# Kernel tuning notes

Hardware: AMD Instinct MI355X
Metric: run time of the kernel (lower is better)

## Reference

```python
import jax, jax.numpy as jnp
import numpy as np
import math

TIN = 4          # patch_size
NF = 128         # num_features
DM = 256         # d_model
NH = 8           # n_heads
HD = DM // NH    # head_dim = 32
FF = 1024        # ff_dim
NL = 4           # num_layers
MAXD = 64        # max_rel_dist -> L = 129


def _ln(x, g, b, eps):
    mu = jnp.mean(x, axis=-1, keepdims=True)
    var = jnp.mean(jnp.square(x - mu), axis=-1, keepdims=True)
    return (x - mu) * jax.lax.rsqrt(var + eps) * g + b


def setup_inputs() -> dict:
    key = jax.random.key(0)
    ks = jax.random.split(key, 24)
    s = 0.02
    d = {
        'x': jax.random.normal(ks[0], (2000, 16, NF), jnp.float32),
        'ln1_g': jnp.ones((TIN * NF,), jnp.float32),
        'ln1_b': jnp.zeros((TIN * NF,), jnp.float32),
        'proj_w': jax.random.normal(ks[1], (TIN * NF, DM), jnp.float32) * s,
        'proj_b': jnp.zeros((DM,), jnp.float32),
        'ln2_g': jnp.ones((DM,), jnp.float32),
        'ln2_b': jnp.zeros((DM,), jnp.float32),
        'rel_bias': jax.random.normal(ks[2], (NH, 2 * MAXD + 1), jnp.float32) * s,
        'ln_attn_g': jnp.ones((NL, DM), jnp.float32),
        'ln_attn_b': jnp.zeros((NL, DM), jnp.float32),
        'qkv_w': jax.random.normal(ks[3], (NL, DM, 3 * DM), jnp.float32) * s,
        'qkv_b': jnp.zeros((NL, 3 * DM), jnp.float32),
        'out_w': jax.random.normal(ks[4], (NL, DM, DM), jnp.float32) * s,
        'out_b': jnp.zeros((NL, DM), jnp.float32),
        'ln_ff_g': jnp.ones((NL, DM), jnp.float32),
        'ln_ff_b': jnp.zeros((NL, DM), jnp.float32),
        'ff1_w': jax.random.normal(ks[5], (NL, DM, FF), jnp.float32) * s,
        'ff1_b': jnp.zeros((NL, FF), jnp.float32),
        'ff2_w': jax.random.normal(ks[6], (NL, FF, DM), jnp.float32) * s,
        'ff2_b': jnp.zeros((NL, DM), jnp.float32),
        'fln_g': jnp.ones((DM,), jnp.float32),
        'fln_b': jnp.zeros((DM,), jnp.float32),
        'op_w': jax.random.normal(ks[7], (DM, NF), jnp.float32) * s,
        'op_b': jnp.zeros((NF,), jnp.float32),
    }
    return d


def reference(x, ln1_g, ln1_b, proj_w, proj_b, ln2_g, ln2_b, rel_bias,
              ln_attn_g, ln_attn_b, qkv_w, qkv_b, out_w, out_b,
              ln_ff_g, ln_ff_b, ff1_w, ff1_b, ff2_w, ff2_b,
              fln_g, fln_b, op_w, op_b):
    # ---- PatchEmbedding ----
    h = jnp.swapaxes(x, 0, 1)                 # [B, T, F]
    B, T, F = h.shape
    n_patch = T // TIN                        # 500 (== chunk_size, single chunk path)
    h = h[:, :n_patch * TIN, :].reshape(B, n_patch, TIN * F)
    h = _ln(h, ln1_g, ln1_b, 1e-6)
    h = h @ proj_w + proj_b
    h = _ln(h, ln2_g, ln2_b, 1e-6)            # [B, S, DM]
    S = n_patch

    # ---- relative position bias [H, S, S] ----
    pos = jnp.arange(S)
    rel = pos[None, :] - pos[:, None]
    idx = jnp.clip(rel, -MAXD, MAXD) + MAXD
    bias = rel_bias[:, idx]                   # [H, S, S]

    # ---- causal mask ----
    causal = jnp.triu(jnp.full((S, S), -jnp.inf, jnp.float32), k=1)
    scale = 1.0 / math.sqrt(HD)

    for l in range(NL):
        # attention block
        a = _ln(h, ln_attn_g[l], ln_attn_b[l], 1e-5)
        qkv = a @ qkv_w[l] + qkv_b[l]         # [B, S, 3*DM]
        q, k, v = jnp.split(qkv, 3, axis=-1)
        q = q.reshape(B, S, NH, HD)
        k = k.reshape(B, S, NH, HD)
        v = v.reshape(B, S, NH, HD)
        scores = jnp.einsum('bihd,bjhd->bhij', q, k) * scale
        scores = scores + bias[None] + causal
        attn = jax.nn.softmax(scores, axis=-1)
        o = jnp.einsum('bhij,bjhd->bihd', attn, v).reshape(B, S, DM)
        h = h + (o @ out_w[l] + out_b[l])
        # ffn block
        f = _ln(h, ln_ff_g[l], ln_ff_b[l], 1e-5)
        f = jax.nn.gelu(f @ ff1_w[l] + ff1_b[l], approximate=False)
        h = h + (f @ ff2_w[l] + ff2_b[l])

    h = _ln(h, fln_g, fln_b, 1e-5)
    h = h @ op_w + op_b                       # [B, S, NF]
    return jnp.swapaxes(h, 0, 1)              # [S, B, NF]
```

## Files before the change

kernel.cpp:

```cpp
#include <hip/hip_runtime.h>

#define TS 500
#define NB 16
#define NROW 8000
#define DMODEL 256
#define NHEAD 8
#define HDIM 32
#define FFD 1024

typedef __bf16 bf16x8 __attribute__((ext_vector_type(8)));
typedef __bf16 bf16x4 __attribute__((ext_vector_type(4)));
typedef float  f32x4  __attribute__((ext_vector_type(4)));
typedef float  f32x2  __attribute__((ext_vector_type(2)));

__device__ __forceinline__ float wred_sum(float v) {
    #pragma unroll
    for (int off = 32; off; off >>= 1) v += __shfl_xor(v, off, 64);
    return v;
}

__device__ __forceinline__ void pa_store(__bf16* __restrict__ PA, int KS,
                                         int grow, int col, float y) {
    int mt = grow >> 4, rl = grow & 15;
    size_t idx = ((size_t)(mt * KS + (col >> 5)) * 64 + ((col >> 3) & 3) * 16 + rl) * 8 + (col & 7);
    PA[idx] = (__bf16)y;
}

__device__ __forceinline__ void ya_store(__bf16* __restrict__ YA,
                                         int lrow, int col, float y) {
    int mtl = lrow >> 4, rl = lrow & 15;
    int idx = (((mtl * 8 + (col >> 5)) * 64) + ((col >> 3) & 3) * 16 + rl) * 8 + (col & 7);
    YA[idx] = (__bf16)y;
}

__global__ __launch_bounds__(256) void k_pack_all(
    const float* __restrict__ qkv_w, const float* __restrict__ out_w,
    const float* __restrict__ ff1_w, const float* __restrict__ ff2_w,
    const float* __restrict__ proj_w, const float* __restrict__ op_w,
    __bf16* __restrict__ PBq, __bf16* __restrict__ PBo,
    __bf16* __restrict__ PB1, __bf16* __restrict__ PB2,
    __bf16* __restrict__ PBp, __bf16* __restrict__ PBop)
{
    int bid = blockIdx.x;
    const float* W; __bf16* PB; int KS, NT, wLS, pLS, l, bx;
    if (bid < 384)       { W = qkv_w;  PB = PBq;  KS = 8;  NT = 48; wLS = 196608; pLS = 196608; l = bid / 96;           bx = bid % 96; }
    else if (bid < 512)  { W = out_w;  PB = PBo;  KS = 8;  NT = 16; wLS = 65536;  pLS = 65536;  l = (bid - 384) / 32;   bx = (bid - 384) % 32; }
    else if (bid < 1024) { W = ff1_w;  PB = PB1;  KS = 8;  NT = 64; wLS = 262144; pLS = 262144; l = (bid - 512) / 128;  bx = (bid - 512) % 128; }
    else if (bid < 1536) { W = ff2_w;  PB = PB2;  KS = 32; NT = 16; wLS = 262144; pLS = 262144; l = (bid - 1024) / 128; bx = (bid - 1024) % 128; }
    else if (bid < 1600) { W = proj_w; PB = PBp;  KS = 16; NT = 16; wLS = 0;      pLS = 0;      l = 0;                  bx = bid - 1536; }
    else                 { W = op_w;   PB = PBop; KS = 8;  NT = 8;  wLS = 0;      pLS = 0;      l = 0;                  bx = bid - 1600; }

    int gid = bx * 256 + threadIdx.x;
    if (gid >= NT * KS * 64) return;
    int lane = gid & 63;
    int ks = (gid >> 6) % KS;
    int nt = (gid >> 6) / KS;
    int N = NT * 16;
    int k0 = ks * 32 + (lane >> 4) * 8;
    int col = nt * 16 + (lane & 15);
    const float* src = W + (size_t)l * wLS;
    bf16x8 v;
    #pragma unroll
    for (int j = 0; j < 8; j++) v[j] = (__bf16)src[(size_t)(k0 + j) * N + col];
    *(bf16x8*)(PB + (size_t)l * pLS + ((size_t)(nt * KS + ks) * 64 + lane) * 8) = v;
}

__global__ __launch_bounds__(256) void k_patchfused(
    const float* __restrict__ x, const float* __restrict__ g1, const float* __restrict__ b1,
    const __bf16* __restrict__ PBp, const float* __restrict__ bias,
    float* __restrict__ h,
    const float* __restrict__ gam, const float* __restrict__ bet,
    const float* __restrict__ gam2, const float* __restrict__ bet2,
    const __bf16* __restrict__ PBq0, const float* __restrict__ qb0,
    __bf16* __restrict__ qkvb)
{
    __shared__ __align__(16) __bf16 As[2][16][64][8];
    __shared__ float redS[4][32];
    __shared__ float redQ[4][32];
    int t = threadIdx.x, lane = t & 63, w = t >> 6;
    int row0 = blockIdx.x * 32;

    for (int rr = 0; rr < 8; rr++) {
        int lrow = w * 8 + rr;
        int row = row0 + lrow;
        int b = row / TS, pp = row - b * TS;
        int kb = lane * 8;
        const float* src = x + ((size_t)(pp * 4 + (kb >> 7)) * NB + b) * 128 + (kb & 127);
        float4 lo = *(const float4*)src;
        float4 hi = *(const float4*)(src + 4);
        float v[8] = {lo.x, lo.y, lo.z, lo.w, hi.x, hi.y, hi.z, hi.w};
        float sm_ = 0.f;
        #pragma unroll
        for (int j = 0; j < 8; j++) sm_ += v[j];
        sm_ = wred_sum(sm_);
        float mu = sm_ * (1.0f / 512.0f);
        float q = 0.f;
        #pragma unroll
        for (int j = 0; j < 8; j++) { float d = v[j] - mu; q += d * d; }
        q = wred_sum(q);
        float rs = rsqrtf(q * (1.0f / 512.0f) + 1e-6f);
        float4 gl = *(const float4*)(g1 + kb), gh = *(const float4*)(g1 + kb + 4);
        float4 bl = *(const float4*)(b1 + kb), bh = *(const float4*)(b1 + kb + 4);
        float gg[8] = {gl.x, gl.y, gl.z, gl.w, gh.x, gh.y, gh.z, gh.w};
        float bbv[8] = {bl.x, bl.y, bl.z, bl.w, bh.x, bh.y, bh.z, bh.w};
        bf16x8 yv;
        #pragma unroll
        for (int j = 0; j < 8; j++) yv[j] = (__bf16)((v[j] - mu) * rs * gg[j] + bbv[j]);
        *(bf16x8*)&As[lrow >> 4][lane >> 2][(lane & 3) * 16 + (lrow & 15)][0] = yv;
    }
    __syncthreads();

    const bf16x8* B8 = (const bf16x8*)PBp;
    f32x4 acc[2][4] = {};
    #pragma unroll 8
    for (int ks = 0; ks < 16; ks++) {
        bf16x8 a0 = *(const bf16x8*)&As[0][ks][lane][0];
        bf16x8 a1 = *(const bf16x8*)&As[1][ks][lane][0];
        #pragma unroll
        for (int n = 0; n < 4; n++) {
            bf16x8 b = B8[((size_t)(w * 4 + n) * 16 + ks) * 64 + lane];
            acc[0][n] = __builtin_amdgcn_mfma_f32_16x16x32_bf16(a0, b, acc[0][n], 0, 0, 0);
            acc[1][n] = __builtin_amdgcn_mfma_f32_16x16x32_bf16(a1, b, acc[1][n], 0, 0, 0);
        }
    }

    int g_ = lane >> 4, cl = lane & 15;
    int rbase = g_ * 4;
    float gamv[4], betv[4], gam2v[4], bet2v[4];
    #pragma unroll
    for (int n = 0; n < 4; n++) {
        int col = (w * 4 + n) * 16 + cl;
        float bv = bias[col];
        gamv[n] = gam[col]; betv[n] = bet[col];
        gam2v[n] = gam2[col]; bet2v[n] = bet2[col];
        #pragma unroll
        for (int m = 0; m < 2; m++)
            #pragma unroll
            for (int r = 0; r < 4; r++) acc[m][n][r] += bv;
    }
    float mu[2][4], rstd[2][4];
    {
        float ps[2][4];
        #pragma unroll
        for (int m = 0; m < 2; m++)
            #pragma unroll
            for (int r = 0; r < 4; r++) {
                float s2 = acc[m][0][r] + acc[m][1][r] + acc[m][2][r] + acc[m][3][r];
                #pragma unroll
                for (int off = 1; off < 16; off <<= 1) s2 += __shfl_xor(s2, off, 64);
                ps[m][r] = s2;
            }
        if (cl == 0)
            #pragma unroll
            for (int m = 0; m < 2; m++)
                #pragma unroll
                for (int r = 0; r < 4; r++) redS[w][m * 16 + rbase + r] = ps[m][r];
        __syncthreads();
        #pragma unroll
        for (int m = 0; m < 2; m++)
            #pragma unroll
            for (int r = 0; r < 4; r++) {
                int lr = m * 16 + rbase + r;
                mu[m][r] = (redS[0][lr] + redS[1][lr] + redS[2][lr] + redS[3][lr]) * (1.0f / 256.0f);
            }
        float pq[2][4];
        #pragma unroll
        for (int m = 0; m < 2; m++)
            #pragma unroll
            for (int r = 0; r < 4; r++) {
                float s2 = 0.f;
                #pragma unroll
                for (int n = 0; n < 4; n++) { float d = acc[m][n][r] - mu[m][r]; s2 += d * d; }
                #pragma unroll
                for (int off = 1; off < 16; off <<= 1) s2 += __shfl_xor(s2, off, 64);
                pq[m][r] = s2;
            }
        if (cl == 0)
            #pragma unroll
            for (int m = 0; m < 2; m++)
                #pragma unroll
                for (int r = 0; r < 4; r++) redQ[w][m * 16 + rbase + r] = pq[m][r];
        __syncthreads();
        #pragma unroll
        for (int m = 0; m < 2; m++)
            #pragma unroll
            for (int r = 0; r < 4; r++) {
                int lr = m * 16 + rbase + r;
                float var = (redQ[0][lr] + redQ[1][lr] + redQ[2][lr] + redQ[3][lr]) * (1.0f / 256.0f);
                rstd[m][r] = rsqrtf(var + 1e-6f);
            }
    }
    float ps2[2][4];
    #pragma unroll
    for (int m = 0; m < 2; m++) {
        int row = row0 + m * 16 + rbase;
        #pragma unroll
        for (int r = 0; r < 4; r++) {
            float s2 = 0.f;
            #pragma unroll
            for (int n = 0; n < 4; n++) {
                int col = (w * 4 + n) * 16 + cl;
                float y1 = (acc[m][n][r] - mu[m][r]) * rstd[m][r] * gamv[n] + betv[n];
                h[(size_t)(row + r) * 256 + col] = y1;
                s2 += y1;
            }
            #pragma unroll
            for (int off = 1; off < 16; off <<= 1) s2 += __shfl_xor(s2, off, 64);
            ps2[m][r] = s2;
        }
    }
    if (cl == 0)
        #pragma unroll
        for (int m = 0; m < 2; m++)
            #pragma unroll
            for (int r = 0; r < 4; r++) redS[w][m * 16 + rbase + r] = ps2[m][r];
    __syncthreads();
    float mu2[2][4], rstd2[2][4];
    #pragma unroll
    for (int m = 0; m < 2; m++)
        #pragma unroll
        for (int r = 0; r < 4; r++) {
            int lr = m * 16 + rbase + r;
            mu2[m][r] = (redS[0][lr] + redS[1][lr] + redS[2][lr] + redS[3][lr]) * (1.0f / 256.0f);
        }
    float pq2[2][4];
    #pragma unroll
    for (int m = 0; m < 2; m++)
        #pragma unroll
        for (int r = 0; r < 4; r++) {
            float s2 = 0.f;
            #pragma unroll
            for (int n = 0; n < 4; n++) {
                float y1 = (acc[m][n][r] - mu[m][r]) * rstd[m][r] * gamv[n] + betv[n];
                float d = y1 - mu2[m][r];
                s2 += d * d;
            }
            #pragma unroll
            for (int off = 1; off < 16; off <<= 1) s2 += __shfl_xor(s2, off, 64);
            pq2[m][r] = s2;
        }
    if (cl == 0)
        #pragma unroll
        for (int m = 0; m < 2; m++)
            #pragma unroll
            for (int r = 0; r < 4; r++) redQ[w][m * 16 + rbase + r] = pq2[m][r];
    __syncthreads();
    #pragma unroll
    for (int m = 0; m < 2; m++)
        #pragma unroll
        for (int r = 0; r < 4; r++) {
            int lr = m * 16 + rbase + r;
            float var = (redQ[0][lr] + redQ[1][lr] + redQ[2][lr] + redQ[3][lr]) * (1.0f / 256.0f);
            rstd2[m][r] = rsqrtf(var + 1e-5f);
        }
    __bf16* YA = &As[0][0][0][0];
    #pragma unroll
    for (int m = 0; m < 2; m++) {
        #pragma unroll
        for (int n = 0; n < 4; n++) {
            int col = (w * 4 + n) * 16 + cl;
            #pragma unroll
            for (int r = 0; r < 4; r++) {
                float y1 = (acc[m][n][r] - mu[m][r]) * rstd[m][r] * gamv[n] + betv[n];
                float y2 = (y1 - mu2[m][r]) * rstd2[m][r] * gam2v[n] + bet2v[n];
                ya_store(YA, m * 16 + rbase + r, col, y2);
            }
        }
    }
    __syncthreads();

    const bf16x8* YA8 = (const bf16x8*)YA;
    const bf16x8* B8q = (const bf16x8*)PBq0;
    for (int m = 0; m < 2; m++) {
        f32x4 acc2[12] = {};
        for (int ks = 0; ks < 8; ks++) {
            bf16x8 a = YA8[(m * 8 + ks) * 64 + lane];
            #pragma unroll
            for (int n = 0; n < 12; n++) {
                bf16x8 b = B8q[((size_t)(w * 12 + n) * 8 + ks) * 64 + lane];
                acc2[n] = __builtin_amdgcn_mfma_f32_16x16x32_bf16(a, b, acc2[n], 0, 0, 0);
            }
        }
        int row = row0 + m * 16 + rbase;
        #pragma unroll
        for (int n = 0; n < 12; n++) {
            int col = (w * 12 + n) * 16 + cl;
            float bv = qb0[col];
            #pragma unroll
            for (int r = 0; r < 4; r++)
                qkvb[(size_t)(row + r) * 768 + col] = (__bf16)(acc2[n][r] + bv);
        }
    }
}

__global__ __launch_bounds__(512) void k_outproj(
    const __bf16* __restrict__ PA, const __bf16* __restrict__ PB,
    const float* __restrict__ bias, float* __restrict__ dst,
    __bf16* __restrict__ dstb,
    const float* __restrict__ gam, const float* __restrict__ bet)
{
    __shared__ float redS[8][16];
    __shared__ float redQ[8][16];
    int t = threadIdx.x, lane = t & 63, w = t >> 6;
    int mt0 = blockIdx.x;

    const bf16x8* A8 = (const bf16x8*)PA;
    const bf16x8* B8 = (const bf16x8*)PB;

    f32x4 acc[2] = {};
    #pragma unroll 8
    for (int ks = 0; ks < 8; ks++) {
        bf16x8 a = A8[((size_t)mt0 * 8 + ks) * 64 + lane];
        #pragma unroll
        for (int n = 0; n < 2; n++) {
            bf16x8 b = B8[((size_t)(w * 2 + n) * 8 + ks) * 64 + lane];
            acc[n] = __builtin_amdgcn_mfma_f32_16x16x32_bf16(a, b, acc[n], 0, 0, 0);
        }
    }

    int g_ = lane >> 4, cl = lane & 15;
    int rbase = g_ * 4;
    float gamv[2], betv[2];
    #pragma unroll
    for (int n = 0; n < 2; n++) {
        int col = (w * 2 + n) * 16 + cl;
        float bv = bias[col];
        gamv[n] = gam[col]; betv[n] = bet[col];
        int row = mt0 * 16 + rbase;
        #pragma unroll
        for (int r = 0; r < 4; r++) {
            float v = acc[n][r] + bv + dst[(size_t)(row + r) * 256 + col];
            dst[(size_t)(row + r) * 256 + col] = v;
            acc[n][r] = v;
        }
    }
    float mu[4], rstd[4];
    {
        float ps[4];
        #pragma unroll
        for (int r = 0; r < 4; r++) {
            float s2 = acc[0][r] + acc[1][r];
            #pragma unroll
            for (int off = 1; off < 16; off <<= 1) s2 += __shfl_xor(s2, off, 64);
            ps[r] = s2;
        }
        if (cl == 0)
            #pragma unroll
            for (int r = 0; r < 4; r++) redS[w][rbase + r] = ps[r];
        __syncthreads();
        #pragma unroll
        for (int r = 0; r < 4; r++) {
            int lr = rbase + r;
            float s2 = 0.f;
            #pragma unroll
            for (int ww = 0; ww < 8; ww++) s2 += redS[ww][lr];
            mu[r] = s2 * (1.0f / 256.0f);
        }
        float pq[4];
        #pragma unroll
        for (int r = 0; r < 4; r++) {
            float s2 = 0.f;
            #pragma unroll
            for (int n = 0; n < 2; n++) { float d = acc[n][r] - mu[r]; s2 += d * d; }
            #pragma unroll
            for (int off = 1; off < 16; off <<= 1) s2 += __shfl_xor(s2, off, 64);
            pq[r] = s2;
        }
        if (cl == 0)
            #pragma unroll
            for (int r = 0; r < 4; r++) redQ[w][rbase + r] = pq[r];
        __syncthreads();
        #pragma unroll
        for (int r = 0; r < 4; r++) {
            int lr = rbase + r;
            float s2 = 0.f;
            #pragma unroll
            for (int ww = 0; ww < 8; ww++) s2 += redQ[ww][lr];
            rstd[r] = rsqrtf(s2 * (1.0f / 256.0f) + 1e-5f);
        }
    }
    int row = mt0 * 16 + rbase;
    #pragma unroll
    for (int n = 0; n < 2; n++) {
        int col = (w * 2 + n) * 16 + cl;
        #pragma unroll
        for (int r = 0; r < 4; r++) {
            float y = (acc[n][r] - mu[r]) * rstd[r] * gamv[n] + betv[n];
            pa_store(dstb, 8, row + r, col, y);
        }
    }
}

template<int MODE>
__global__ __launch_bounds__(512) void k_fffused(
    const __bf16* __restrict__ PA, const __bf16* __restrict__ PB1,
    const float* __restrict__ b1, const __bf16* __restrict__ PB2,
    const float* __restrict__ b2, float* __restrict__ h,
    const float* __restrict__ gam, const float* __restrict__ bet,
    const __bf16* __restrict__ PBn, const float* __restrict__ bn,
    __bf16* __restrict__ qkvb, float* __restrict__ outp)
{
    __shared__ __align__(16) __bf16 F1T[1024][16];
    __shared__ float redS[8][16];
    __shared__ float redQ[8][16];
    int t = threadIdx.x, lane = t & 63, w = t >> 6;
    int mt = blockIdx.x;
    int g_ = lane >> 4, cl = lane & 15, rbase = g_ * 4;

    const bf16x8* A8 = (const bf16x8*)PA;
    const bf16x8* B81 = (const bf16x8*)PB1;
    const bf16x8* B82 = (const bf16x8*)PB2;

    f32x4 acc1[8] = {};
    #pragma unroll 2
    for (int ks = 0; ks < 8; ks++) {
        bf16x8 a = A8[((size_t)mt * 8 + ks) * 64 + lane];
        #pragma unroll
        for (int n = 0; n < 8; n++) {
            bf16x8 b = B81[((size_t)(w * 8 + n) * 8 + ks) * 64 + lane];
            acc1[n] = __builtin_amdgcn_mfma_f32_16x16x32_bf16(a, b, acc1[n], 0, 0, 0);
        }
    }
    #pragma unroll
    for (int n = 0; n < 8; n++) {
        int col = (w * 8 + n) * 16 + cl;
        float bv = b1[col];
        bf16x4 pv;
        #pragma unroll
        for (int r = 0; r < 4; r++) {
            float xx = acc1[n][r] + bv;
            pv[r] = (__bf16)(0.5f * xx * (1.0f + erff(xx * 0.70710678118654752f)));
        }
        *(bf16x4*)&F1T[col][rbase] = pv;
    }
    __syncthreads();

    f32x4 acc[2] = {};
    for (int kb = 0; kb < 8; kb++) {
        f32x2 lo[4], hi[4];
        #pragma unroll
        for (int q = 0; q < 4; q++) {
            unsigned ta = (unsigned)(uintptr_t)&F1T[(kb * 4 + q) * 32 + 8 * g_][0] + cl * 8;
            asm volatile("ds_read_b64_tr_b16 %0, %1" : "=v"(lo[q]) : "v"(ta) : "memory");
            asm volatile("ds_read_b64_tr_b16 %0, %1 offset:128" : "=v"(hi[q]) : "v"(ta) : "memory");
        }
        asm volatile("s_waitcnt lgkmcnt(0)" ::: "memory");
        __builtin_amdgcn_sched_barrier(0);
        #pragma unroll
        for (int q = 0; q < 4; q++) {
            int ks = kb * 4 + q;
            f32x4 pc = {lo[q][0], lo[q][1], hi[q][0], hi[q][1]};
            bf16x8 a = __builtin_bit_cast(bf16x8, pc);
            #pragma unroll
            for (int n = 0; n < 2; n++) {
                bf16x8 b = B82[((size_t)(w * 2 + n) * 32 + ks) * 64 + lane];
                acc[n] = __builtin_amdgcn_mfma_f32_16x16x32_bf16(a, b, acc[n], 0, 0, 0);
            }
        }
    }

    float gamv[2], betv[2];
    #pragma unroll
    for (int n = 0; n < 2; n++) {
        int col = (w * 2 + n) * 16 + cl;
        float bv = b2[col];
        gamv[n] = gam[col]; betv[n] = bet[col];
        int row = mt * 16 + rbase;
        #pragma unroll
        for (int r = 0; r < 4; r++) {
            float v = acc[n][r] + bv + h[(size_t)(row + r) * 256 + col];
            h[(size_t)(row + r) * 256 + col] = v;
            acc[n][r] = v;
        }
    }
    float mu[4], rstd[4];
    {
        float ps[4];
        #pragma unroll
        for (int r = 0; r < 4; r++) {
            float s2 = acc[0][r] + acc[1][r];
            #pragma unroll
            for (int off = 1; off < 16; off <<= 1) s2 += __shfl_xor(s2, off, 64);
            ps[r] = s2;
        }
        if (cl == 0)
            #pragma unroll
            for (int r = 0; r < 4; r++) redS[w][rbase + r] = ps[r];
        __syncthreads();
        #pragma unroll
        for (int r = 0; r < 4; r++) {
            int lr = rbase + r;
            float s2 = 0.f;
            #pragma unroll
            for (int ww = 0; ww < 8; ww++) s2 += redS[ww][lr];
            mu[r] = s2 * (1.0f / 256.0f);
        }
        float pq[4];
        #pragma unroll
        for (int r = 0; r < 4; r++) {
            float s2 = 0.f;
            #pragma unroll
            for (int n = 0; n < 2; n++) { float d = acc[n][r] - mu[r]; s2 += d * d; }
            #pragma unroll
            for (int off = 1; off < 16; off <<= 1) s2 += __shfl_xor(s2, off, 64);
            pq[r] = s2;
        }
        if (cl == 0)
            #pragma unroll
            for (int r = 0; r < 4; r++) redQ[w][rbase + r] = pq[r];
        __syncthreads();
        #pragma unroll
        for (int r = 0; r < 4; r++) {
            int lr = rbase + r;
            float s2 = 0.f;
            #pragma unroll
            for (int ww = 0; ww < 8; ww++) s2 += redQ[ww][lr];
            rstd[r] = rsqrtf(s2 * (1.0f / 256.0f) + 1e-5f);
        }
    }
    __bf16* YA = &F1T[0][0];
    #pragma unroll
    for (int n = 0; n < 2; n++) {
        int col = (w * 2 + n) * 16 + cl;
        #pragma unroll
        for (int r = 0; r < 4; r++) {
            float y = (acc[n][r] - mu[r]) * rstd[r] * gamv[n] + betv[n];
            ya_store(YA, rbase + r, col, y);
        }
    }
    __syncthreads();

    const bf16x8* YA8 = (const bf16x8*)YA;
    const bf16x8* B8n = (const bf16x8*)PBn;
    if constexpr (MODE == 0) {
        f32x4 acc2[6] = {};
        for (int ks = 0; ks < 8; ks++) {
            bf16x8 a = YA8[ks * 64 + lane];
            #pragma unroll
            for (int n = 0; n < 6; n++) {
                bf16x8 b = B8n[((size_t)(w * 6 + n) * 8 + ks) * 64 + lane];
                acc2[n] = __builtin_amdgcn_mfma_f32_16x16x32_bf16(a, b, acc2[n], 0, 0, 0);
            }
        }
        int row = mt * 16 + rbase;
        #pragma unroll
        for (int n = 0; n < 6; n++) {
            int col = (w * 6 + n) * 16 + cl;
            float bv = bn[col];
            #pragma unroll
            for (int r = 0; r < 4; r++)
                qkvb[(size_t)(row + r) * 768 + col] = (__bf16)(acc2[n][r] + bv);
        }
    } else {
        f32x4 acc2 = {};
        #pragma unroll 4
        for (int ks = 0; ks < 8; ks++) {
            bf16x8 a = YA8[ks * 64 + lane];
            bf16x8 b = B8n[((size_t)w * 8 + ks) * 64 + lane];
            acc2 = __builtin_amdgcn_mfma_f32_16x16x32_bf16(a, b, acc2, 0, 0, 0);
        }
        int row = mt * 16 + rbase;
        int col = w * 16 + cl;
        float bv = bn[col];
        #pragma unroll
        for (int r = 0; r < 4; r++) {
            int grow = row + r;
            int bq = grow / TS, pp = grow - bq * TS;
            outp[((size_t)pp * NB + bq) * 128 + col] = acc2[r] + bv;
        }
    }
}

__global__ __launch_bounds__(256) void k_attn(
    const __bf16* __restrict__ qkv, const float* __restrict__ rel_bias,
    __bf16* __restrict__ PA)
{
    __shared__ __align__(16) __bf16 Kfr[4][64][8];
    __shared__ __align__(16) __bf16 Vpl[2][64][16];
    __shared__ __align__(16) __bf16 PT[4][64][16];
    __shared__ float bias_s[132];

    int bh = blockIdx.x, qt = 7 - blockIdx.y;
    int b = bh >> 3, hh = bh & 7;
    int q0 = qt * 64;
    int t = threadIdx.x, lane = t & 63, w = t >> 6;
    int c = lane & 15, g = lane >> 4;

    const __bf16* base = qkv + (size_t)b * TS * 768 + hh * 32;

    if (t < 129) bias_s[t] = rel_bias[hh * 129 + t];

    bf16x8 aq = {};
    {
        int qi = q0 + 16 * w + c;
        if (qi < TS) aq = *(const bf16x8*)(base + (size_t)qi * 768 + 8 * g);
    }

    float lpart[4] = {0.f, 0.f, 0.f, 0.f};
    f32x4 O0 = {}, O1 = {};
    const float scale = 0.17677669529663687f;

    int nj = qt + 1;

    for (int it = 0; it < nj; it++) {
        int j0 = it * 64;
        __syncthreads();
        {
            int j = j0 + w * 16 + c;
            bf16x8 kv = {};
            if (j < TS) kv = *(const bf16x8*)(base + (size_t)j * 768 + 256 + 8 * g);
            *(bf16x8*)&Kfr[w][lane][0] = kv;
        }
        {
            int jl = t >> 2, dseg = t & 3;
            int j = j0 + jl;
            bf16x8 vv = {};
            if (j < TS) vv = *(const bf16x8*)(base + (size_t)j * 768 + 512 + 8 * dseg);
            *(bf16x8*)&Vpl[dseg >> 1][jl][(dseg & 1) * 8] = vv;
        }
        __syncthreads();

        f32x4 S[4];
        f32x4 zero = {};
        #pragma unroll
        for (int jt = 0; jt < 4; jt++) {
            bf16x8 bk = *(const bf16x8*)&Kfr[jt][lane][0];
            S[jt] = __builtin_amdgcn_mfma_f32_16x16x32_bf16(aq, bk, zero, 0, 0, 0);
        }

        #pragma unroll
        for (int jt = 0; jt < 4; jt++) {
            int j = j0 + jt * 16 + c;
            #pragma unroll
            for (int r = 0; r < 4; r++) {
                int i = q0 + 16 * w + 4 * g + r;
                int rel = j - i;
                rel = rel < -64 ? -64 : (rel > 64 ? 64 : rel);
                float sv = S[jt][r] * scale + bias_s[rel + 64];
                float pr = (j > i) ? 0.f : __expf(sv);
                S[jt][r] = pr;
                lpart[r] += pr;
            }
        }

        #pragma unroll
        for (int jt = 0; jt < 4; jt++) {
            bf16x4 pv;
            pv[0] = (__bf16)S[jt][0]; pv[1] = (__bf16)S[jt][1];
            pv[2] = (__bf16)S[jt][2]; pv[3] = (__bf16)S[jt][3];
            *(bf16x4*)&PT[w][jt * 16 + c][4 * g] = pv;
        }
        asm volatile("s_waitcnt lgkmcnt(0)" ::: "memory");
        __builtin_amdgcn_sched_barrier(0);

        f32x2 pa_lo[2], pa_hi[2], vb_lo[2][2], vb_hi[2][2];
        #pragma unroll
        for (int jb = 0; jb < 2; jb++) {
            unsigned pta = (unsigned)(uintptr_t)&PT[w][jb * 32 + 8 * g][0] + c * 8;
            asm volatile("ds_read_b64_tr_b16 %0, %1" : "=v"(pa_lo[jb]) : "v"(pta) : "memory");
            asm volatile("ds_read_b64_tr_b16 %0, %1 offset:128" : "=v"(pa_hi[jb]) : "v"(pta) : "memory");
            #pragma unroll
            for (int dh = 0; dh < 2; dh++) {
                unsigned vta = (unsigned)(uintptr_t)&Vpl[dh][jb * 32 + 8 * g][0] + c * 8;
                asm volatile("ds_read_b64_tr_b16 %0, %1" : "=v"(vb_lo[jb][dh]) : "v"(vta) : "memory");
                asm volatile("ds_read_b64_tr_b16 %0, %1 offset:128" : "=v"(vb_hi[jb][dh]) : "v"(vta) : "memory");
            }
        }
        asm volatile("s_waitcnt lgkmcnt(0)" ::: "memory");
        __builtin_amdgcn_sched_barrier(0);

        #pragma unroll
        for (int jb = 0; jb < 2; jb++) {
            f32x4 pc = {pa_lo[jb][0], pa_lo[jb][1], pa_hi[jb][0], pa_hi[jb][1]};
            bf16x8 pa = __builtin_bit_cast(bf16x8, pc);
            f32x4 v0c = {vb_lo[jb][0][0], vb_lo[jb][0][1], vb_hi[jb][0][0], vb_hi[jb][0][1]};
            f32x4 v1c = {vb_lo[jb][1][0], vb_lo[jb][1][1], vb_hi[jb][1][0], vb_hi[jb][1][1]};
            bf16x8 vb0 = __builtin_bit_cast(bf16x8, v0c);
            bf16x8 vb1 = __builtin_bit_cast(bf16x8, v1c);
            O0 = __builtin_amdgcn_mfma_f32_16x16x32_bf16(pa, vb0, O0, 0, 0, 0);
            O1 = __builtin_amdgcn_mfma_f32_16x16x32_bf16(pa, vb1, O1, 0, 0, 0);
        }
    }

    #pragma unroll
    for (int r = 0; r < 4; r++) {
        #pragma unroll
        for (int off = 1; off < 16; off <<= 1) lpart[r] += __shfl_xor(lpart[r], off, 64);
    }
    #pragma unroll
    for (int r = 0; r < 4; r++) {
        int i = q0 + 16 * w + 4 * g + r;
        if (i < TS) {
            float inv = 1.0f / lpart[r];
            int grow = b * TS + i;
            int mt = grow >> 4, rl = grow & 15;
            size_t fb = (size_t)(mt * 8 + hh) * 64;
            PA[(fb + ((c >> 3) & 1) * 16 + rl) * 8 + (c & 7)]       = (__bf16)(O0[r] * inv);
            PA[(fb + (2 + ((c >> 3) & 1)) * 16 + rl) * 8 + (c & 7)] = (__bf16)(O1[r] * inv);
        }
    }
}

extern "C" void kernel_launch(void* const* d_in, const int* in_sizes, int n_in,
                              void* d_out, int out_size, void* d_ws, size_t ws_size,
                              hipStream_t stream)
{
    const float* x        = (const float*)d_in[0];
    const float* ln1_g    = (const float*)d_in[1];
    const float* ln1_b    = (const float*)d_in[2];
    const float* proj_w   = (const float*)d_in[3];
    const float* proj_b   = (const float*)d_in[4];
    const float* ln2_g    = (const float*)d_in[5];
    const float* ln2_b    = (const float*)d_in[6];
    const float* rel_bias = (const float*)d_in[7];
    const float* ln_attn_g= (const float*)d_in[8];
    const float* ln_attn_b= (const float*)d_in[9];
    const float* qkv_w    = (const float*)d_in[10];
    const float* qkv_b    = (const float*)d_in[11];
    const float* out_w    = (const float*)d_in[12];
    const float* out_b    = (const float*)d_in[13];
    const float* ln_ff_g  = (const float*)d_in[14];
    const float* ln_ff_b  = (const float*)d_in[15];
    const float* ff1_w    = (const float*)d_in[16];
    const float* ff1_b    = (const float*)d_in[17];
    const float* ff2_w    = (const float*)d_in[18];
    const float* ff2_b    = (const float*)d_in[19];
    const float* fln_g    = (const float*)d_in[20];
    const float* fln_b    = (const float*)d_in[21];
    const float* op_w     = (const float*)d_in[22];
    const float* op_b     = (const float*)d_in[23];
    float* out = (float*)d_out;

    char* ws = (char*)d_ws;
    float*  h     = (float*)(ws);
    __bf16* qkvb  = (__bf16*)(ws + 8192000);
    __bf16* PA    = (__bf16*)(ws + 20480000);
    __bf16* PBq   = (__bf16*)(ws + 24576000);
    __bf16* PBo   = (__bf16*)(ws + 26148864);
    __bf16* PB1   = (__bf16*)(ws + 26673152);
    __bf16* PB2   = (__bf16*)(ws + 28770304);
    __bf16* PBp   = (__bf16*)(ws + 30867456);
    __bf16* PBop  = (__bf16*)(ws + 31129600);

    k_pack_all<<<1616, 256, 0, stream>>>(qkv_w, out_w, ff1_w, ff2_w, proj_w, op_w,
                                         PBq, PBo, PB1, PB2, PBp, PBop);

    k_patchfused<<<250, 256, 0, stream>>>(x, ln1_g, ln1_b, PBp, proj_b, h,
                                          ln2_g, ln2_b, ln_attn_g, ln_attn_b,
                                          PBq, qkv_b, qkvb);

    for (int l = 0; l < 4; l++) {
        dim3 ag(NB * NHEAD, 8);
        k_attn<<<ag, 256, 0, stream>>>(qkvb, rel_bias, PA);
        k_outproj<<<500, 512, 0, stream>>>(PA, PBo + (size_t)l * 65536, out_b + l * 256,
                                           h, PA, ln_ff_g + l * 256, ln_ff_b + l * 256);
        if (l < 3) {
            k_fffused<0><<<500, 512, 0, stream>>>(PA, PB1 + (size_t)l * 262144, ff1_b + l * 1024,
                                                  PB2 + (size_t)l * 262144, ff2_b + l * 256, h,
                                                  ln_attn_g + (l + 1) * 256, ln_attn_b + (l + 1) * 256,
                                                  PBq + (size_t)(l + 1) * 196608, qkv_b + (l + 1) * 768,
                                                  qkvb, nullptr);
        } else {
            k_fffused<1><<<500, 512, 0, stream>>>(PA, PB1 + (size_t)l * 262144, ff1_b + l * 1024,
                                                  PB2 + (size_t)l * 262144, ff2_b + l * 256, h,
                                                  fln_g, fln_b,
                                                  PBop, op_b, nullptr, out);
        }
    }
}
```

Measured before the change: 285.3 us.

## Share K/V tiles between two adjacent query tiles per attention block

Each attention block now has 512 threads covering two adjacent 64-row query tiles (pr pairs qt=2pr and 2pr+1), so every K/V tile staged in shared memory is reused by 8 waves rather than 4. The grid halves, and loading is split so waves 0-3 stage K while waves 4-7 stage V. This cuts redundant global reads of K/V and removes half the block launches. In exchange, the lower query tile idles for one iteration and the larger blocks have a coarser causal load balance.

```diff
diff --git a/kernel.cpp b/kernel.cpp
--- a/kernel.cpp
+++ b/kernel.cpp
@@ -571,19 +571,22 @@
     }
 }
 
-__global__ __launch_bounds__(256) void k_attn(
+__global__ __launch_bounds__(512) void k_attn(
     const __bf16* __restrict__ qkv, const float* __restrict__ rel_bias,
     __bf16* __restrict__ PA)
 {
     __shared__ __align__(16) __bf16 Kfr[4][64][8];
     __shared__ __align__(16) __bf16 Vpl[2][64][16];
-    __shared__ __align__(16) __bf16 PT[4][64][16];
+    __shared__ __align__(16) __bf16 PT[8][64][16];
     __shared__ float bias_s[132];
 
-    int bh = blockIdx.x, qt = 7 - blockIdx.y;
+    int bh = blockIdx.x;
+    int pr = 3 - blockIdx.y;
     int b = bh >> 3, hh = bh & 7;
-    int q0 = qt * 64;
     int t = threadIdx.x, lane = t & 63, w = t >> 6;
+    int wg = w & 3, grp = w >> 2;
+    int qt = 2 * pr + 1 - grp;
+    int q0 = qt * 64 + wg * 16;
     int c = lane & 15, g = lane >> 4;
 
     const __bf16* base = qkv + (size_t)b * TS * 768 + hh * 32;
@@ -592,7 +595,7 @@
 
     bf16x8 aq = {};
     {
-        int qi = q0 + 16 * w + c;
+        int qi = q0 + c;
         if (qi < TS) aq = *(const bf16x8*)(base + (size_t)qi * 768 + 8 * g);
     }
 
@@ -600,19 +603,19 @@
     f32x4 O0 = {}, O1 = {};
     const float scale = 0.17677669529663687f;
 
-    int nj = qt + 1;
+    int nj = 2 * pr + 2;
 
     for (int it = 0; it < nj; it++) {
         int j0 = it * 64;
         __syncthreads();
-        {
+        if (w < 4) {
             int j = j0 + w * 16 + c;
             bf16x8 kv = {};
             if (j < TS) kv = *(const bf16x8*)(base + (size_t)j * 768 + 256 + 8 * g);
             *(bf16x8*)&Kfr[w][lane][0] = kv;
-        }
-        {
-            int jl = t >> 2, dseg = t & 3;
+        } else {
+            int t2 = t - 256;
+            int jl = t2 >> 2, dseg = t2 & 3;
             int j = j0 + jl;
             bf16x8 vv = {};
             if (j < TS) vv = *(const bf16x8*)(base + (size_t)j * 768 + 512 + 8 * dseg);
@@ -620,6 +623,8 @@
         }
         __syncthreads();
 
+        if (it > qt) continue;
+
         f32x4 S[4];
         f32x4 zero = {};
         #pragma unroll
@@ -633,13 +638,13 @@
             int j = j0 + jt * 16 + c;
             #pragma unroll
             for (int r = 0; r < 4; r++) {
-                int i = q0 + 16 * w + 4 * g + r;
+                int i = q0 + 4 * g + r;
                 int rel = j - i;
                 rel = rel < -64 ? -64 : (rel > 64 ? 64 : rel);
                 float sv = S[jt][r] * scale + bias_s[rel + 64];
-                float pr = (j > i) ? 0.f : __expf(sv);
-                S[jt][r] = pr;
-                lpart[r] += pr;
+                float pr_ = (j > i) ? 0.f : __expf(sv);
+                S[jt][r] = pr_;
+                lpart[r] += pr_;
             }
         }
 
@@ -689,7 +694,7 @@
     }
     #pragma unroll
     for (int r = 0; r < 4; r++) {
-        int i = q0 + 16 * w + 4 * g + r;
+        int i = q0 + 4 * g + r;
         if (i < TS) {
             float inv = 1.0f / lpart[r];
             int grow = b * TS + i;
@@ -750,8 +755,8 @@
                                           PBq, qkv_b, qkvb);
 
     for (int l = 0; l < 4; l++) {
-        dim3 ag(NB * NHEAD, 8);
-        k_attn<<<ag, 256, 0, stream>>>(qkvb, rel_bias, PA);
+        dim3 ag(NB * NHEAD, 4);
+        k_attn<<<ag, 512, 0, stream>>>(qkvb, rel_bias, PA);
         k_outproj<<<500, 512, 0, stream>>>(PA, PBo + (size_t)l * 65536, out_b + l * 256,
                                            h, PA, ln_ff_g + l * 256, ln_ff_b + l * 256);
         if (l < 3) {
```

After: 280.0 us. Within noise of the previous version (-1.9%).
